# Kernel optimization log

Hardware: AMD Instinct MI355X
Metric: run time of the kernel (lower is better)

The kernel has to match this reference:

```python
import jax, jax.numpy as jnp
import numpy as np

N_CLASS = 50257
EMB = 1024
HID = 1024
BATCH = 1024  # must equal HID due to the module's [H,H] zero state init
SEQ = 128


def setup_inputs() -> dict:
    key = jax.random.key(0)
    ks = jax.random.split(key, 8)
    s_e = 1.0 / np.sqrt(EMB)
    s_h = 1.0 / np.sqrt(HID)
    X = jax.random.randint(ks[0], (BATCH, SEQ), 0, N_CLASS, dtype=jnp.int32)
    C = jax.random.normal(ks[1], (N_CLASS, EMB), dtype=jnp.float32)
    # gate order along last axis: i, f, g, o (each block of size HID)
    Wx = jax.random.uniform(ks[2], (EMB, 4 * HID), jnp.float32, -s_e, s_e)
    bx = jax.random.uniform(ks[3], (4 * HID,), jnp.float32, -s_e, s_e)
    Wh = jax.random.uniform(ks[4], (HID, 4 * HID), jnp.float32, -s_h, s_h)
    bh = jax.random.uniform(ks[5], (4 * HID,), jnp.float32, -s_h, s_h)
    W_out = jax.random.uniform(ks[6], (HID, N_CLASS), jnp.float32, -s_h, s_h)
    b_out = jnp.ones((N_CLASS,), dtype=jnp.float32)  # nn.Parameter(torch.ones)
    return {"X": X, "C": C, "Wx": Wx, "bx": bx, "Wh": Wh, "bh": bh,
            "W_out": W_out, "b_out": b_out}


def _lstm_last_hidden(xs, Wx, bx, Wh, bh):
    # xs: [S, B, E]; with zero-initialized h/c of shape [H,H] and B == H,
    # the original broadcast-buggy code reduces to a standard LSTM.
    x_proj = jnp.einsum('sbe,eg->sbg', xs, Wx) + bx  # [S, B, 4H]
    B = xs.shape[1]
    H = Wh.shape[0]
    h0 = jnp.zeros((B, H), dtype=xs.dtype)
    c0 = jnp.zeros((B, H), dtype=xs.dtype)

    def step(carry, xp):
        h, c = carry
        gates = xp + h @ Wh + bh  # [B, 4H]
        i, f, g, o = jnp.split(gates, 4, axis=-1)
        i = jax.nn.sigmoid(i)
        f = jax.nn.sigmoid(f)
        g = jnp.tanh(g)
        o = jax.nn.sigmoid(o)
        c = f * c + i * g
        h = o * jnp.tanh(c)
        return (h, c), None

    (h, _), _ = jax.lax.scan(step, (h0, c0), x_proj)
    return h  # [B, H] last timestep hidden


def reference(X, C, Wx, bx, Wh, bh, W_out, b_out):
    emb = C[X]                      # [B, S, E]
    xs = jnp.swapaxes(emb, 0, 1)    # [S, B, E]  (transpose(0,1))
    h_last = _lstm_last_hidden(xs, Wx, bx, Wh, bh)
    return h_last @ W_out + b_out   # [B, n_class]
```

## Files before the change

### kernel.cpp

```cpp
#include <hip/hip_runtime.h>
#include <hip/hip_bf16.h>

#define SEQ_   128
#define NCLS_  50257
#define EMB_   1024
#define HID_   1024
#define BATCH_ 1024
#define G4_    4096

typedef __attribute__((ext_vector_type(8))) short short8;
typedef __attribute__((ext_vector_type(4))) float f32x4;

__device__ __forceinline__ void async_copy16(void* lds, const void* g) {
  __builtin_amdgcn_global_load_lds(
      (const __attribute__((address_space(1))) void*)g,
      (__attribute__((address_space(3))) void*)lds, 16, 0, 0);
}

__device__ __forceinline__ void mfma_acc(f32x4& c, const short8& a, const short8& b) {
  asm("v_mfma_f32_16x16x32_bf16 %0, %1, %2, %0" : "+v"(c) : "v"(a), "v"(b));
}

__device__ __forceinline__ float sigmoidf_(float x) {
  return 1.f / (1.f + __expf(-x));
}
__device__ __forceinline__ float tanhf_(float x) {
  x = fminf(12.f, fmaxf(-12.f, x));
  float e = __expf(2.f * x);
  return (e - 1.f) / (e + 1.f);
}
__device__ __forceinline__ float bf2f_(ushort u) {
  return __uint_as_float(((unsigned int)u) << 16);
}

template <int EPI>
__global__ __launch_bounds__(256) void gemm_bt(
    const __hip_bfloat16* __restrict__ A, const __hip_bfloat16* __restrict__ Bt,
    float* __restrict__ outF, __hip_bfloat16* __restrict__ outB,
    int Mreal, int Nreal, int K, long ostride,
    const float* __restrict__ bias0) {
  __shared__ __align__(16) char smem[65536];

  const int tid = threadIdx.x;
  const int lane = tid & 63;
  const int w = tid >> 6;
  const int wm = w >> 1;
  const int wn = w & 1;
  const int m0 = blockIdx.y * 128;
  const int n0 = blockIdx.x * 128;

  const int fr = lane & 15;
  const int kb = (lane >> 4) * 16;
  const int swz = (fr & 7) << 4;

  f32x4 acc[4][4];
#pragma unroll
  for (int i = 0; i < 4; ++i)
#pragma unroll
    for (int j = 0; j < 4; ++j) acc[i][j] = (f32x4)(0.0f);

  auto STAGE = [&](int kc, int b) {
#pragma unroll
    for (int q = 0; q < 8; ++q) {
      const int ridx = (q & 3) * 256 + tid;
      const int row = ridx >> 3;
      const int ch = ridx & 7;
      const __hip_bfloat16* src;
      char* dst;
      if (q < 4) {
        long ar = m0 + row; if (ar >= Mreal) ar = Mreal - 1;
        src = A + ar * (long)K + kc * 64 + ch * 8;
        dst = smem + b * 16384 + ridx * 16;
      } else {
        long br = n0 + row; if (br >= Nreal) br = Nreal - 1;
        src = Bt + br * (long)K + kc * 64 + ch * 8;
        dst = smem + 32768 + b * 16384 + ridx * 16;
      }
      async_copy16(dst, src);
    }
  };

  const int KC = K >> 6;
  STAGE(0, 0);
  for (int kc = 0; kc < KC; ++kc) {
    const int b = kc & 1;
    if (kc + 1 < KC) {
      STAGE(kc + 1, b ^ 1);
      asm volatile("s_waitcnt vmcnt(8)" ::: "memory");
    } else {
      asm volatile("s_waitcnt vmcnt(0)" ::: "memory");
    }
    __builtin_amdgcn_s_barrier();
    __builtin_amdgcn_sched_barrier(0);

    short8 aR[2][4], bR[2][4];
#pragma unroll
    for (int kk = 0; kk < 2; ++kk)
#pragma unroll
      for (int f = 0; f < 4; ++f) {
        aR[kk][f] = *(const short8*)(smem + b * 16384 +
                     (wm * 64 + f * 16 + fr) * 128 + ((kk * 64 + kb) ^ swz));
        bR[kk][f] = *(const short8*)(smem + 32768 + b * 16384 +
                     (wn * 64 + f * 16 + fr) * 128 + ((kk * 64 + kb) ^ swz));
      }
#pragma unroll
    for (int fm = 0; fm < 4; ++fm)
#pragma unroll
      for (int fn = 0; fn < 4; ++fn) {
        mfma_acc(acc[fm][fn], aR[0][fm], bR[0][fn]);
        mfma_acc(acc[fm][fn], aR[1][fm], bR[1][fn]);
      }
    __builtin_amdgcn_sched_barrier(0);
    __builtin_amdgcn_s_barrier();
  }

  const int cn = lane & 15;
  const int rb = (lane >> 4) * 4;
#pragma unroll
  for (int fn = 0; fn < 4; ++fn) {
    const int col = n0 + wn * 64 + fn * 16 + cn;
    const float badd = (col < Nreal) ? bias0[col] : 0.f;
#pragma unroll
    for (int fm = 0; fm < 4; ++fm) {
#pragma unroll
      for (int r = 0; r < 4; ++r) {
        const int row = m0 + wm * 64 + fm * 16 + rb + r;
        const float v = acc[fm][fn][r] + badd;
        if (EPI == 0) {
          if (row < Mreal) outB[(long)row * ostride + col] = __float2bfloat16(v);
        } else {
          if (col < Nreal && row < Mreal) outF[(long)row * ostride + col] = v;
        }
      }
    }
  }
}

__global__ __launch_bounds__(256) void lstm_step(
    const __hip_bfloat16* __restrict__ hprev,
    const __hip_bfloat16* __restrict__ Whs,
    const __hip_bfloat16* __restrict__ Epr,
    const int* __restrict__ X,
    float* __restrict__ cbuf,
    __hip_bfloat16* __restrict__ hnext,
    __hip_bfloat16* __restrict__ hfin,
    int t, int last) {
  __shared__ __align__(16) char smem[65536];

  const int tid = threadIdx.x;
  const int lane = tid & 63;
  const int w = tid >> 6;
  const int wm = w >> 1;
  const int wn = w & 1;
  const int bid = blockIdx.x;
  const int xcd = bid & 7;
  const int j = bid >> 3;
  const int ht = xcd * 4 + (j & 3);
  const int mt = j >> 2;
  const int m0 = mt * 128;
  const int h0 = ht * 32;

  const int fr = lane & 15;
  const int cn = lane & 15;
  const int rb = (lane >> 4) * 4;
  const int kb = (lane >> 4) * 16;
  const int swz = (fr & 7) << 4;
  const int hcol = h0 + wn * 16 + cn;

  int tok[16];
#pragma unroll
  for (int fm = 0; fm < 4; ++fm)
#pragma unroll
    for (int r = 0; r < 4; ++r) {
      const int row = m0 + wm * 64 + fm * 16 + rb + r;
      tok[fm * 4 + r] = X[row * SEQ_ + t];
    }
  ushort4 ep[16];
  float cold[16];
#pragma unroll
  for (int fm = 0; fm < 4; ++fm)
#pragma unroll
    for (int r = 0; r < 4; ++r) {
      const int idx = fm * 4 + r;
      const int row = m0 + wm * 64 + fm * 16 + rb + r;
      ep[idx] = *(const ushort4*)(Epr + (size_t)tok[idx] * G4_ + 4 * hcol);
      cold[idx] = cbuf[(size_t)row * HID_ + hcol];
    }

  f32x4 acc[4][4];
#pragma unroll
  for (int i = 0; i < 4; ++i)
#pragma unroll
    for (int g = 0; g < 4; ++g) acc[i][g] = (f32x4)(0.0f);

  auto STAGE = [&](int kc, int b) {
#pragma unroll
    for (int q = 0; q < 8; ++q) {
      const int ridx = (q & 3) * 256 + tid;
      const int row = ridx >> 3;
      const int ch = ridx & 7;
      const __hip_bfloat16* src;
      char* dst;
      if (q < 4) {
        src = hprev + (size_t)(m0 + row) * HID_ + kc * 64 + ch * 8;
        dst = smem + b * 16384 + ridx * 16;
      } else {
        const int g = row >> 5, hh = row & 31;
        src = Whs + (size_t)(g * 1024 + h0 + hh) * HID_ + kc * 64 + ch * 8;
        dst = smem + 32768 + b * 16384 + ridx * 16;
      }
      async_copy16(dst, src);
    }
  };

  STAGE(0, 0);
  for (int kc = 0; kc < 16; ++kc) {
    const int b = kc & 1;
    if (kc < 15) {
      STAGE(kc + 1, b ^ 1);
      asm volatile("s_waitcnt vmcnt(8)" ::: "memory");
    } else {
      asm volatile("s_waitcnt vmcnt(0)" ::: "memory");
    }
    __builtin_amdgcn_s_barrier();
    __builtin_amdgcn_sched_barrier(0);

    short8 aR[2][4], bR[2][4];
#pragma unroll
    for (int kk = 0; kk < 2; ++kk)
#pragma unroll
      for (int f = 0; f < 4; ++f) {
        aR[kk][f] = *(const short8*)(smem + b * 16384 +
                     (wm * 64 + f * 16 + fr) * 128 + ((kk * 64 + kb) ^ swz));
        bR[kk][f] = *(const short8*)(smem + 32768 + b * 16384 +
                     (f * 32 + wn * 16 + fr) * 128 + ((kk * 64 + kb) ^ swz));
      }
#pragma unroll
    for (int fm = 0; fm < 4; ++fm)
#pragma unroll
      for (int g = 0; g < 4; ++g) {
        mfma_acc(acc[fm][g], aR[0][fm], bR[0][g]);
        mfma_acc(acc[fm][g], aR[1][fm], bR[1][g]);
      }
    __builtin_amdgcn_sched_barrier(0);
    __builtin_amdgcn_s_barrier();
  }

#pragma unroll
  for (int fm = 0; fm < 4; ++fm) {
#pragma unroll
    for (int r = 0; r < 4; ++r) {
      const int idx = fm * 4 + r;
      const int row = m0 + wm * 64 + fm * 16 + rb + r;
      const float iv = sigmoidf_(acc[fm][0][r] + bf2f_(ep[idx].x));
      const float fv = sigmoidf_(acc[fm][1][r] + bf2f_(ep[idx].y));
      const float gv = tanhf_(acc[fm][2][r] + bf2f_(ep[idx].z));
      const float ov = sigmoidf_(acc[fm][3][r] + bf2f_(ep[idx].w));
      const float cv = fv * cold[idx] + iv * gv;
      cbuf[(size_t)row * HID_ + hcol] = cv;
      const float hval = ov * tanhf_(cv);
      const __hip_bfloat16 hb = __float2bfloat16(hval);
      const int hsw = (hcol & ~63) | ((hcol & 63) ^ ((row & 7) << 3));
      hnext[(size_t)row * HID_ + hsw] = hb;
      if (last) hfin[(size_t)row * HID_ + hsw] = hb;
    }
  }
}

template <bool SWZ>
__global__ __launch_bounds__(256) void conv_bf16_k(const float* __restrict__ in,
                                                   __hip_bfloat16* __restrict__ out, int n4) {
  const int i = blockIdx.x * 256 + threadIdx.x;
  if (i >= n4) return;
  const float4 v = ((const float4*)in)[i];
  int o = i * 4;
  if (SWZ) {
    const int row = o >> 10, col = o & 1023;
    const int cs = (col & ~63) | ((col & 63) ^ ((row & 7) << 3));
    o = (o & ~1023) | cs;
  }
  out[o + 0] = __float2bfloat16(v.x);
  out[o + 1] = __float2bfloat16(v.y);
  out[o + 2] = __float2bfloat16(v.z);
  out[o + 3] = __float2bfloat16(v.w);
}

template <bool PERM, bool SWZ>
__global__ __launch_bounds__(256) void transpose_conv(const float* __restrict__ in,
                                                      __hip_bfloat16* __restrict__ out,
                                                      int R, int C) {
  __shared__ float tile[32][33];
  const int c0 = blockIdx.x * 32, r0 = blockIdx.y * 32;
  const int tx = threadIdx.x, ty = threadIdx.y;
#pragma unroll
  for (int i = 0; i < 4; ++i) {
    const int r = r0 + ty + i * 8, cc = c0 + tx;
    tile[ty + i * 8][tx] = (r < R && cc < C) ? in[(size_t)r * C + cc] : 0.f;
  }
  __syncthreads();
#pragma unroll
  for (int i = 0; i < 4; ++i) {
    const int ro = c0 + ty + i * 8, co = r0 + tx;
    if (ro < C && co < R) {
      const int n = PERM ? ((ro & 1023) * 4 + (ro >> 10)) : ro;
      int k = co;
      if (SWZ) k = (k & ~63) | ((k & 63) ^ ((n & 7) << 3));
      out[(size_t)n * R + k] = __float2bfloat16(tile[tx][ty + i * 8]);
    }
  }
}

__global__ __launch_bounds__(256) void bias_perm(const float* __restrict__ bx,
                                                 const float* __restrict__ bh,
                                                 float* __restrict__ bP) {
  const int n = blockIdx.x * 256 + threadIdx.x;
  if (n >= G4_) return;
  const int h = n >> 2, g = n & 3;
  bP[n] = bx[g * HID_ + h] + bh[g * HID_ + h];
}

extern "C" void kernel_launch(void* const* d_in, const int* in_sizes, int n_in,
                              void* d_out, int out_size, void* d_ws, size_t ws_size,
                              hipStream_t stream) {
  const int* X = (const int*)d_in[0];
  const float* C = (const float*)d_in[1];
  const float* Wx = (const float*)d_in[2];
  const float* bx = (const float*)d_in[3];
  const float* Wh = (const float*)d_in[4];
  const float* bh = (const float*)d_in[5];
  const float* Wo = (const float*)d_in[6];
  const float* bo = (const float*)d_in[7];
  float* out = (float*)d_out;

  char* p = (char*)d_ws;
  const size_t szCb  = (size_t)NCLS_ * EMB_ * 2;
  const size_t szWxt = (size_t)G4_ * EMB_ * 2;
  const size_t szWhs = (size_t)G4_ * HID_ * 2;
  const size_t szEpr = (size_t)NCLS_ * G4_ * 2;
  const size_t szH   = (size_t)BATCH_ * HID_ * 2;
  const size_t szC   = (size_t)BATCH_ * HID_ * 4;
  const size_t szBp  = (size_t)G4_ * 4;
  if (ws_size < szCb + szWxt + szWhs + szEpr + 3 * szH + szC + szBp) return;

  __hip_bfloat16* Cb   = (__hip_bfloat16*)p; p += szCb;
  __hip_bfloat16* WxtP = (__hip_bfloat16*)p; p += szWxt;
  __hip_bfloat16* Whs  = (__hip_bfloat16*)p; p += szWhs;
  __hip_bfloat16* Epr  = (__hip_bfloat16*)p; p += szEpr;
  __hip_bfloat16* hA   = (__hip_bfloat16*)p; p += szH;
  __hip_bfloat16* hB   = (__hip_bfloat16*)p; p += szH;
  __hip_bfloat16* hfin = (__hip_bfloat16*)p; p += szH;
  float* cbuf          = (float*)p;          p += szC;
  float* bP            = (float*)p;          p += szBp;

  {
    const int n4 = NCLS_ * EMB_ / 4;
    conv_bf16_k<true><<<(n4 + 255) / 256, 256, 0, stream>>>(C, Cb, n4);
  }
  transpose_conv<true, true><<<dim3(G4_ / 32, EMB_ / 32), dim3(32, 8), 0, stream>>>(
      Wx, WxtP, EMB_, G4_);
  transpose_conv<false, true><<<dim3(G4_ / 32, HID_ / 32), dim3(32, 8), 0, stream>>>(
      Wh, Whs, HID_, G4_);
  bias_perm<<<G4_ / 256, 256, 0, stream>>>(bx, bh, bP);

  gemm_bt<0><<<dim3(G4_ / 128, (NCLS_ + 127) / 128), 256, 0, stream>>>(
      Cb, WxtP, nullptr, Epr, NCLS_, G4_, EMB_, G4_, bP);

  hipMemsetAsync(hA, 0, szH, stream);
  hipMemsetAsync(cbuf, 0, szC, stream);

  for (int t = 0; t < SEQ_; ++t) {
    const __hip_bfloat16* hp = (t & 1) ? hB : hA;
    __hip_bfloat16* hn = (t & 1) ? hA : hB;
    lstm_step<<<256, 256, 0, stream>>>(hp, Whs, Epr, X, cbuf, hn, hfin, t,
                                       (int)(t == SEQ_ - 1));
  }

  __hip_bfloat16* Wot = Cb;
  transpose_conv<false, true><<<dim3((NCLS_ + 31) / 32, HID_ / 32), dim3(32, 8), 0,
                                stream>>>(Wo, Wot, HID_, NCLS_);

  gemm_bt<2><<<dim3((NCLS_ + 127) / 128, BATCH_ / 128), 256, 0, stream>>>(
      hfin, Wot, out, nullptr, BATCH_, NCLS_, HID_, NCLS_, bo);
}
```

Measured before the change: 3.307 ms.

## Split LSTM step K-loop across two wave groups with LDS reduction

Doubles the lstm_step block to 512 threads. Two groups of four waves each take half of the K dimension, so the serial K loop drops from 16 to 8 iterations. Partial gate sums are combined through LDS, and the epilogue is reorganised so each thread handles 8 contiguous hidden columns of one row, with vectorized stores of c and h. The cost is 128KB of dynamic LDS per block, an extra reduction pass with two barriers, and higher register and LDS pressure that could limit occupancy.

```diff
diff --git a/kernel.cpp b/kernel.cpp
--- a/kernel.cpp
+++ b/kernel.cpp
@@ -136,7 +136,7 @@
   }
 }
 
-__global__ __launch_bounds__(256) void lstm_step(
+__global__ __launch_bounds__(512) void lstm_step(
     const __hip_bfloat16* __restrict__ hprev,
     const __hip_bfloat16* __restrict__ Whs,
     const __hip_bfloat16* __restrict__ Epr,
@@ -145,13 +145,15 @@
     __hip_bfloat16* __restrict__ hnext,
     __hip_bfloat16* __restrict__ hfin,
     int t, int last) {
-  __shared__ __align__(16) char smem[65536];
+  extern __shared__ __align__(16) char smem[];
+  float* gacc = (float*)smem;
 
   const int tid = threadIdx.x;
   const int lane = tid & 63;
   const int w = tid >> 6;
-  const int wm = w >> 1;
+  const int wm = (w >> 1) & 1;
   const int wn = w & 1;
+  const int kh = w >> 2;
   const int bid = blockIdx.x;
   const int xcd = bid & 7;
   const int j = bid >> 3;
@@ -161,31 +163,20 @@
   const int h0 = ht * 32;
 
   const int fr = lane & 15;
-  const int cn = lane & 15;
-  const int rb = (lane >> 4) * 4;
   const int kb = (lane >> 4) * 16;
   const int swz = (fr & 7) << 4;
-  const int hcol = h0 + wn * 16 + cn;
-
-  int tok[16];
-#pragma unroll
-  for (int fm = 0; fm < 4; ++fm)
-#pragma unroll
-    for (int r = 0; r < 4; ++r) {
-      const int row = m0 + wm * 64 + fm * 16 + rb + r;
-      tok[fm * 4 + r] = X[row * SEQ_ + t];
-    }
-  ushort4 ep[16];
-  float cold[16];
-#pragma unroll
-  for (int fm = 0; fm < 4; ++fm)
-#pragma unroll
-    for (int r = 0; r < 4; ++r) {
-      const int idx = fm * 4 + r;
-      const int row = m0 + wm * 64 + fm * 16 + rb + r;
-      ep[idx] = *(const ushort4*)(Epr + (size_t)tok[idx] * G4_ + 4 * hcol);
-      cold[idx] = cbuf[(size_t)row * HID_ + hcol];
-    }
+
+  const int crow = tid >> 2;
+  const int hq = tid & 3;
+  const int prow = m0 + crow;
+  const int tok1 = X[prow * SEQ_ + t];
+  ushort4 ep[8];
+  float cold[8];
+#pragma unroll
+  for (int jj = 0; jj < 8; ++jj) {
+    ep[jj] = *(const ushort4*)(Epr + (size_t)tok1 * G4_ + (h0 + hq * 8 + jj) * 4);
+    cold[jj] = cbuf[(size_t)prow * HID_ + h0 + hq * 8 + jj];
+  }
 
   f32x4 acc[4][4];
 #pragma unroll
@@ -196,27 +187,26 @@
   auto STAGE = [&](int kc, int b) {
 #pragma unroll
     for (int q = 0; q < 8; ++q) {
-      const int ridx = (q & 3) * 256 + tid;
-      const int row = ridx >> 3;
-      const int ch = ridx & 7;
+      const int region = q >> 1;
+      const int r = (q & 1) * 512 + tid;
+      const int row = r >> 3;
+      const int ch = r & 7;
       const __hip_bfloat16* src;
-      char* dst;
-      if (q < 4) {
-        src = hprev + (size_t)(m0 + row) * HID_ + kc * 64 + ch * 8;
-        dst = smem + b * 16384 + ridx * 16;
+      if (region < 2) {
+        src = hprev + (size_t)(m0 + row) * HID_ + region * 512 + kc * 64 + ch * 8;
       } else {
         const int g = row >> 5, hh = row & 31;
-        src = Whs + (size_t)(g * 1024 + h0 + hh) * HID_ + kc * 64 + ch * 8;
-        dst = smem + 32768 + b * 16384 + ridx * 16;
-      }
-      async_copy16(dst, src);
+        src = Whs + (size_t)(g * 1024 + h0 + hh) * HID_ + (region - 2) * 512 +
+              kc * 64 + ch * 8;
+      }
+      async_copy16(smem + region * 32768 + b * 16384 + r * 16, src);
     }
   };
 
   STAGE(0, 0);
-  for (int kc = 0; kc < 16; ++kc) {
+  for (int kc = 0; kc < 8; ++kc) {
     const int b = kc & 1;
-    if (kc < 15) {
+    if (kc < 7) {
       STAGE(kc + 1, b ^ 1);
       asm volatile("s_waitcnt vmcnt(8)" ::: "memory");
     } else {
@@ -225,15 +215,17 @@
     __builtin_amdgcn_s_barrier();
     __builtin_amdgcn_sched_barrier(0);
 
+    const char* baseA = smem + kh * 32768 + b * 16384;
+    const char* baseB = smem + 65536 + kh * 32768 + b * 16384;
     short8 aR[2][4], bR[2][4];
 #pragma unroll
     for (int kk = 0; kk < 2; ++kk)
 #pragma unroll
       for (int f = 0; f < 4; ++f) {
-        aR[kk][f] = *(const short8*)(smem + b * 16384 +
-                     (wm * 64 + f * 16 + fr) * 128 + ((kk * 64 + kb) ^ swz));
-        bR[kk][f] = *(const short8*)(smem + 32768 + b * 16384 +
-                     (f * 32 + wn * 16 + fr) * 128 + ((kk * 64 + kb) ^ swz));
+        aR[kk][f] = *(const short8*)(baseA + (wm * 64 + f * 16 + fr) * 128 +
+                                     ((kk * 64 + kb) ^ swz));
+        bR[kk][f] = *(const short8*)(baseB + (f * 32 + wn * 16 + fr) * 128 +
+                                     ((kk * 64 + kb) ^ swz));
       }
 #pragma unroll
     for (int fm = 0; fm < 4; ++fm)
@@ -246,25 +238,54 @@
     __builtin_amdgcn_s_barrier();
   }
 
-#pragma unroll
-  for (int fm = 0; fm < 4; ++fm) {
-#pragma unroll
-    for (int r = 0; r < 4; ++r) {
-      const int idx = fm * 4 + r;
-      const int row = m0 + wm * 64 + fm * 16 + rb + r;
-      const float iv = sigmoidf_(acc[fm][0][r] + bf2f_(ep[idx].x));
-      const float fv = sigmoidf_(acc[fm][1][r] + bf2f_(ep[idx].y));
-      const float gv = tanhf_(acc[fm][2][r] + bf2f_(ep[idx].z));
-      const float ov = sigmoidf_(acc[fm][3][r] + bf2f_(ep[idx].w));
-      const float cv = fv * cold[idx] + iv * gv;
-      cbuf[(size_t)row * HID_ + hcol] = cv;
-      const float hval = ov * tanhf_(cv);
-      const __hip_bfloat16 hb = __float2bfloat16(hval);
-      const int hsw = (hcol & ~63) | ((hcol & 63) ^ ((row & 7) << 3));
-      hnext[(size_t)row * HID_ + hsw] = hb;
-      if (last) hfin[(size_t)row * HID_ + hsw] = hb;
-    }
-  }
+  const int cn = lane & 15;
+  const int rb = (lane >> 4) * 4;
+  if (kh == 0) {
+#pragma unroll
+    for (int fm = 0; fm < 4; ++fm)
+#pragma unroll
+      for (int g = 0; g < 4; ++g)
+#pragma unroll
+        for (int r = 0; r < 4; ++r)
+          gacc[(wm * 64 + fm * 16 + rb + r) * 132 + (wn * 16 + cn) * 4 + g] =
+              acc[fm][g][r];
+  }
+  __syncthreads();
+  if (kh == 1) {
+#pragma unroll
+    for (int fm = 0; fm < 4; ++fm)
+#pragma unroll
+      for (int g = 0; g < 4; ++g)
+#pragma unroll
+        for (int r = 0; r < 4; ++r)
+          gacc[(wm * 64 + fm * 16 + rb + r) * 132 + (wn * 16 + cn) * 4 + g] +=
+              acc[fm][g][r];
+  }
+  __syncthreads();
+
+  const float* gr = gacc + crow * 132 + hq * 32;
+  f32x4 cnew0, cnew1;
+  short8 hv;
+#pragma unroll
+  for (int jj = 0; jj < 8; ++jj) {
+    const f32x4 g4 = *(const f32x4*)(gr + jj * 4);
+    const float iv = sigmoidf_(g4[0] + bf2f_(ep[jj].x));
+    const float fv = sigmoidf_(g4[1] + bf2f_(ep[jj].y));
+    const float gv = tanhf_(g4[2] + bf2f_(ep[jj].z));
+    const float ov = sigmoidf_(g4[3] + bf2f_(ep[jj].w));
+    const float cv = fv * cold[jj] + iv * gv;
+    if (jj < 4) cnew0[jj] = cv; else cnew1[jj - 4] = cv;
+    const float hval = ov * tanhf_(cv);
+    const __hip_bfloat16 hb = __float2bfloat16(hval);
+    hv[jj] = *reinterpret_cast<const short*>(&hb);
+  }
+  float* cdst = cbuf + (size_t)prow * HID_ + h0 + hq * 8;
+  *(f32x4*)cdst = cnew0;
+  *(f32x4*)(cdst + 4) = cnew1;
+  const int hcolb = h0 + hq * 8;
+  const int hswb = (hcolb & ~63) | ((hcolb & 63) ^ ((prow & 7) << 3));
+  *(short8*)(hnext + (size_t)prow * HID_ + hswb) = hv;
+  if (last) *(short8*)(hfin + (size_t)prow * HID_ + hswb) = hv;
 }
 
 template <bool SWZ>
@@ -371,8 +392,8 @@
   for (int t = 0; t < SEQ_; ++t) {
     const __hip_bfloat16* hp = (t & 1) ? hB : hA;
     __hip_bfloat16* hn = (t & 1) ? hA : hB;
-    lstm_step<<<256, 256, 0, stream>>>(hp, Whs, Epr, X, cbuf, hn, hfin, t,
-                                       (int)(t == SEQ_ - 1));
+    lstm_step<<<256, 512, 131072, stream>>>(hp, Whs, Epr, X, cbuf, hn, hfin, t,
+                                            (int)(t == SEQ_ - 1));
   }
 
   __hip_bfloat16* Wot = Cb;
```

Result: no change. 3.306 ms (-0.0%).
